# Performance work log

Measured on AMD Instinct MI355X. Metric: run time of the kernel, lower is better.

Reference implementation:

```python
import jax, jax.numpy as jnp
import numpy as np

DIM = 512
HEADS = 8
DH = 64          # dim_head = 512 // 8
M = 256          # num_landmarks = 512 // 2
PINV_ITERS = 6
N_PATCH = 40000
IN_DIM = 1024
NUM_CLASSES = 2
GRID = 200       # ceil(sqrt(40000)) -> exact square, add_length = 0


def layernorm(x, w, b, eps=1e-5):
    mu = x.mean(-1, keepdims=True)
    var = ((x - mu) ** 2).mean(-1, keepdims=True)
    return (x - mu) * jax.lax.rsqrt(var + eps) * w + b


def moore_penrose_pinv(x, iters=PINV_ITERS):
    # lucidrains nystrom-attention iterative pseudoinverse
    ax = jnp.abs(x)
    z = jnp.swapaxes(x, -1, -2) / (jnp.max(ax.sum(-1)) * jnp.max(ax.sum(-2)))
    I = jnp.eye(x.shape[-1], dtype=x.dtype)
    for _ in range(iters):
        xz = x @ z
        z = 0.25 * z @ (13 * I - xz @ (15 * I - xz @ (7 * I - xz)))
    return z


def depthwise_conv2d(x, w, pad):
    # x: (B,C,H,W); w: (C,1,kh,kw) torch-style OIHW depthwise kernel
    return jax.lax.conv_general_dilated(
        x, w, (1, 1), [(pad[0], pad[0]), (pad[1], pad[1])],
        dimension_numbers=('NCHW', 'OIHW', 'NCHW'),
        feature_group_count=x.shape[1])


def nystrom_attention(x, qkv_w, out_w, out_b, res_w):
    b, n, _ = x.shape
    pad = (M - n % M) % M
    xp = jnp.pad(x, ((0, 0), (pad, 0), (0, 0)))   # pad at FRONT of sequence
    N = n + pad
    qkv = xp @ qkv_w                              # (b,N,3*h*d), no bias
    q, k, v = jnp.split(qkv, 3, axis=-1)
    to_heads = lambda t: t.reshape(b, N, HEADS, DH).transpose(0, 2, 1, 3)
    q, k, v = to_heads(q), to_heads(k), to_heads(v)
    q = q * (DH ** -0.5)
    l = N // M
    q_l = q.reshape(b, HEADS, M, l, DH).mean(axis=3)   # (b,h,m,d) landmarks
    k_l = k.reshape(b, HEADS, M, l, DH).mean(axis=3)
    attn1 = jax.nn.softmax(jnp.einsum('bhid,bhjd->bhij', q, k_l), axis=-1)   # (b,h,N,m)
    attn2 = jax.nn.softmax(jnp.einsum('bhid,bhjd->bhij', q_l, k_l), axis=-1)  # (b,h,m,m)
    attn3 = jax.nn.softmax(jnp.einsum('bhid,bhjd->bhij', q_l, k), axis=-1)   # (b,h,m,N)
    out = (attn1 @ moore_penrose_pinv(attn2)) @ (attn3 @ v)                   # (b,h,N,d)
    out = out + depthwise_conv2d(v, res_w, (16, 0))    # residual depthwise conv (kernel 33x1)
    out = out.transpose(0, 2, 1, 3).reshape(b, N, HEADS * DH)[:, -n:]
    return out @ out_w + out_b


def ppeg(x, w7, b7, w5, b5, w3, b3, H, W):
    B, _, C = x.shape
    cls_t, feat = x[:, :1], x[:, 1:]
    f = feat.transpose(0, 2, 1).reshape(B, C, H, W)
    y = (f
         + depthwise_conv2d(f, w7, (3, 3)) + b7[None, :, None, None]
         + depthwise_conv2d(f, w5, (2, 2)) + b5[None, :, None, None]
         + depthwise_conv2d(f, w3, (1, 1)) + b3[None, :, None, None])
    y = y.reshape(B, C, H * W).transpose(0, 2, 1)
    return jnp.concatenate([cls_t, y], axis=1)


def setup_inputs() -> dict:
    key = jax.random.key(0)
    ks = iter(jax.random.split(key, 32))
    r = lambda shape, s=0.02: jax.random.normal(next(ks), shape, dtype=jnp.float32) * s
    inp = {
        'x': jax.random.normal(next(ks), (1, N_PATCH, IN_DIM), dtype=jnp.float32),
        'fc1_w': r((IN_DIM, DIM)), 'fc1_b': jnp.zeros((DIM,), jnp.float32),
        'cls_token': r((1, 1, DIM), 1e-6),
        'l1_norm_w': jnp.ones((DIM,), jnp.float32), 'l1_norm_b': jnp.zeros((DIM,), jnp.float32),
        'l1_qkv_w': r((DIM, 3 * HEADS * DH)), 'l1_out_w': r((HEADS * DH, DIM)),
        'l1_out_b': jnp.zeros((DIM,), jnp.float32), 'l1_res_w': r((HEADS, 1, 33, 1)),
        'p7_w': r((DIM, 1, 7, 7)), 'p7_b': jnp.zeros((DIM,), jnp.float32),
        'p5_w': r((DIM, 1, 5, 5)), 'p5_b': jnp.zeros((DIM,), jnp.float32),
        'p3_w': r((DIM, 1, 3, 3)), 'p3_b': jnp.zeros((DIM,), jnp.float32),
        'l2_norm_w': jnp.ones((DIM,), jnp.float32), 'l2_norm_b': jnp.zeros((DIM,), jnp.float32),
        'l2_qkv_w': r((DIM, 3 * HEADS * DH)), 'l2_out_w': r((HEADS * DH, DIM)),
        'l2_out_b': jnp.zeros((DIM,), jnp.float32), 'l2_res_w': r((HEADS, 1, 33, 1)),
        'norm_w': jnp.ones((DIM,), jnp.float32), 'norm_b': jnp.zeros((DIM,), jnp.float32),
        'fc2_w': r((DIM, NUM_CLASSES)), 'fc2_b': jnp.zeros((NUM_CLASSES,), jnp.float32),
    }
    return inp


def reference(x, fc1_w, fc1_b, cls_token,
              l1_norm_w, l1_norm_b, l1_qkv_w, l1_out_w, l1_out_b, l1_res_w,
              p7_w, p7_b, p5_w, p5_b, p3_w, p3_b,
              l2_norm_w, l2_norm_b, l2_qkv_w, l2_out_w, l2_out_b, l2_res_w,
              norm_w, norm_b, fc2_w, fc2_b):
    # _fc1: Linear + ReLU (dropout inactive at eval)
    h = jax.nn.relu(x @ fc1_w + fc1_b)            # (1, 40000, 512)
    # 40000 = 200*200 -> add_length = 0, no square padding needed
    B = h.shape[0]
    h = jnp.concatenate([jnp.broadcast_to(cls_token, (B, 1, DIM)), h], axis=1)
    # layer1: pre-norm Nystrom attention with residual
    h = h + nystrom_attention(layernorm(h, l1_norm_w, l1_norm_b), l1_qkv_w, l1_out_w, l1_out_b, l1_res_w)
    # PPEG positional mixing on the 200x200 token grid
    h = ppeg(h, p7_w, p7_b, p5_w, p5_b, p3_w, p3_b, GRID, GRID)
    # layer2
    h = h + nystrom_attention(layernorm(h, l2_norm_w, l2_norm_b), l2_qkv_w, l2_out_w, l2_out_b, l2_res_w)
    h = layernorm(h, norm_w, norm_b)
    cls_out = h[:, 0]
    logits = cls_out @ fc2_w + fc2_b              # (1, num_classes)
    return logits
```

## Files before the change

kernel.cpp:

```cpp
#include <hip/hip_runtime.h>
#include <hip/hip_bf16.h>

#define DIMC   512
#define HEADS  8
#define DH     64
#define MLM    256
#define NPATCH 40000
#define NTOK   40001
#define PADF   191
#define NSEQ   40192
#define NSEQP  40224
#define LWIN   157
#define INDIM  1024
#define GRID   200
#define CHUNKS 64
#define PER    628

typedef _Float16 h8 __attribute__((ext_vector_type(8)));
typedef _Float16 h4 __attribute__((ext_vector_type(4)));
typedef float    f4 __attribute__((ext_vector_type(4)));

#define WAVE_LDS_FENCE() asm volatile("s_waitcnt lgkmcnt(0)" ::: "memory")

__device__ __forceinline__ void gl_lds(const _Float16* g, _Float16* l) {
  __builtin_amdgcn_global_load_lds(
      (const __attribute__((address_space(1))) void*)g,
      (__attribute__((address_space(3))) void*)l, 16, 0, 0);
}

template<int NW, bool ISMAX>
__device__ __forceinline__ float blkRed(float v, float* s) {
  #pragma unroll
  for (int o = 32; o; o >>= 1) {
    float t = __shfl_down(v, o, 64);
    v = ISMAX ? fmaxf(v, t) : v + t;
  }
  int lane = threadIdx.x & 63, w = threadIdx.x >> 6;
  __syncthreads();
  if (lane == 0) s[w] = v;
  __syncthreads();
  float r = s[0];
  #pragma unroll
  for (int i = 1; i < NW; i++) r = ISMAX ? fmaxf(r, s[i]) : r + s[i];
  return r;
}

__global__ __launch_bounds__(512)
void k_set_cls(const float* __restrict__ cls, float* __restrict__ h) {
  h[threadIdx.x] = cls[threadIdx.x];
}

__global__ __launch_bounds__(256)
void k_f32_to_f16(const float* __restrict__ in, _Float16* __restrict__ out) {
  int i = blockIdx.x * 256 + threadIdx.x;
  float4 v = ((const float4*)in)[i];
  h4 o = {(_Float16)v.x, (_Float16)v.y, (_Float16)v.z, (_Float16)v.w};
  *(h4*)(out + (size_t)i * 4) = o;
}

__global__ __launch_bounds__(256)
void k_zpad(_Float16* q16, _Float16* k16, _Float16* v16) {
  int idx = blockIdx.x * 256 + threadIdx.x;
  int h = idx >> 11, r = (idx >> 6) & 31, d = idx & 63;
  size_t a = ((size_t)h * NSEQP + NSEQ + r) * 64 + d;
  q16[a] = (_Float16)0.f; k16[a] = (_Float16)0.f; v16[a] = (_Float16)0.f;
}

__global__ __launch_bounds__(256)
void k_wt16(const float* __restrict__ B, _Float16* __restrict__ Bt, int K, int N)
{
  __shared__ float tile[32][33];
  int kb = blockIdx.x * 32, nb = blockIdx.y * 32;
  int x = threadIdx.x & 31, y0 = threadIdx.x >> 5;
  #pragma unroll
  for (int yy = y0; yy < 32; yy += 8)
    tile[yy][x] = B[(size_t)(kb + yy) * N + nb + x];
  __syncthreads();
  #pragma unroll
  for (int yy = y0; yy < 32; yy += 8)
    Bt[(size_t)(nb + yy) * K + kb + x] = (_Float16)tile[x][yy];
}

__global__ __launch_bounds__(256)
void k_gemm16(const _Float16* __restrict__ A, const _Float16* __restrict__ Bt,
              const float* __restrict__ bias, float* __restrict__ C,
              _Float16* __restrict__ q16, _Float16* __restrict__ k16, _Float16* __restrict__ v16,
              int Mr, int K, int N, int flags)
{
  __shared__ __attribute__((aligned(16))) _Float16 As[128 * 32];
  __shared__ __attribute__((aligned(16))) _Float16 Bs[128 * 32];
  int bm = blockIdx.x * 128, bn = blockIdx.y * 128;
  int t = threadIdx.x;
  int lane = t & 63, w = t >> 6;
  int wm = (w >> 1) * 64, wn = (w & 1) * 64;
  int r = lane & 15, q = lane >> 4;
  int sub = lane >> 2;
  int kq = (lane & 3) * 8;

  const f4 zero = {0.f, 0.f, 0.f, 0.f};
  f4 acc[4][4];
  #pragma unroll
  for (int mi = 0; mi < 4; mi++)
    #pragma unroll
    for (int nj = 0; nj < 4; nj++) acc[mi][nj] = zero;

  for (int k0 = 0; k0 < K; k0 += 32) {
    #pragma unroll
    for (int c = 0; c < 2; c++) {
      int rowA = (w * 2 + c) * 16 + sub;
      int gmA = bm + rowA; if (gmA > Mr - 1) gmA = Mr - 1;
      gl_lds(A  + (size_t)gmA * K + k0 + kq,          As + (w * 2 + c) * 512);
      gl_lds(Bt + (size_t)(bn + rowA) * K + k0 + kq,  Bs + (w * 2 + c) * 512);
    }
    __syncthreads();
    h8 af[4], bf[4];
    #pragma unroll
    for (int i = 0; i < 4; i++) {
      af[i] = *(const h8*)(As + (wm + i * 16 + r) * 32 + q * 8);
      bf[i] = *(const h8*)(Bs + (wn + i * 16 + r) * 32 + q * 8);
    }
    #pragma unroll
    for (int mi = 0; mi < 4; mi++)
      #pragma unroll
      for (int nj = 0; nj < 4; nj++)
        acc[mi][nj] = __builtin_amdgcn_mfma_f32_16x16x32_f16(af[mi], bf[nj], acc[mi][nj], 0, 0, 0);
    __syncthreads();
  }
  #pragma unroll
  for (int mi = 0; mi < 4; mi++) {
    #pragma unroll
    for (int i = 0; i < 4; i++) {
      int gm = bm + wm + mi * 16 + q * 4 + i;
      if (gm >= Mr) continue;
      #pragma unroll
      for (int nj = 0; nj < 4; nj++) {
        int gn = bn + wn + nj * 16 + r;
        float v = acc[mi][nj][i];
        if (flags & 4) {
          int which = gn >> 9, hh = (gn >> 6) & 7, dd = gn & 63;
          _Float16* dst = (which == 0) ? q16 : (which == 1) ? k16 : v16;
          dst[((size_t)hh * NSEQP + gm) * 64 + dd] = (_Float16)v;
        } else {
          if (bias) v += bias[gn];
          if (flags & 2) v += C[(size_t)gm * N + gn];
          if (flags & 1) v = fmaxf(v, 0.f);
          C[(size_t)gm * N + gn] = v;
        }
      }
    }
  }
}

__global__ __launch_bounds__(256)
void k_ln_pad(const float* __restrict__ h, const float* __restrict__ w,
              const float* __restrict__ b, _Float16* __restrict__ xln)
{
  __shared__ float sbuf[8];
  int t = blockIdx.x;
  int tid = threadIdx.x;
  _Float16* out = xln + (size_t)t * DIMC;
  if (t < PADF) { out[tid] = (_Float16)0.f; out[tid + 256] = (_Float16)0.f; return; }
  const float* row = h + (size_t)(t - PADF) * DIMC;
  float x0 = row[tid], x1 = row[tid + 256];
  float mu = blkRed<4,false>(x0 + x1, sbuf) * (1.f / 512.f);
  float d0 = x0 - mu, d1 = x1 - mu;
  float var = blkRed<4,false>(d0 * d0 + d1 * d1, sbuf) * (1.f / 512.f);
  float rstd = rsqrtf(var + 1e-5f);
  out[tid]       = (_Float16)(d0 * rstd * w[tid]       + b[tid]);
  out[tid + 256] = (_Float16)(d1 * rstd * w[tid + 256] + b[tid + 256]);
}

__global__ __launch_bounds__(256)
void k_vt(const _Float16* __restrict__ v16, _Float16* __restrict__ vt16)
{
  __shared__ _Float16 tl[64][72];
  int h = blockIdx.y;
  int t0 = blockIdx.x * 64;
  for (int c = threadIdx.x; c < 512; c += 256) {
    int row = c >> 3, ch = (c & 7) * 8;
    h8 v = {};
    if (t0 + row < NSEQP)
      v = *(const h8*)(v16 + ((size_t)h * NSEQP + t0 + row) * 64 + ch);
    *(h8*)&tl[row][ch] = v;
  }
  __syncthreads();
  int d = threadIdx.x & 63, tg = (threadIdx.x >> 6) * 16;
  if (t0 + tg < NSEQP) {
    _Float16 tmp[16];
    #pragma unroll
    for (int k = 0; k < 16; k++) tmp[k] = tl[tg + k][d];
    *(h8*)(vt16 + ((size_t)h * 64 + d) * NSEQP + t0 + tg)     = *(h8*)tmp;
    *(h8*)(vt16 + ((size_t)h * 64 + d) * NSEQP + t0 + tg + 8) = *(h8*)(tmp + 8);
  }
}

__global__ __launch_bounds__(256)
void k_landmarks(const _Float16* __restrict__ q16, const _Float16* __restrict__ k16,
                 float* __restrict__ ql, float* __restrict__ kl,
                 _Float16* __restrict__ ql16, _Float16* __restrict__ kl16)
{
  __shared__ float red[2][16][64];
  int h = blockIdx.x >> 8, i = blockIdx.x & 255;
  int jg = threadIdx.x >> 4, d4 = (threadIdx.x & 15) * 4;
  const _Float16* qb = q16 + ((size_t)h * NSEQP + i * LWIN) * 64;
  const _Float16* kb = k16 + ((size_t)h * NSEQP + i * LWIN) * 64;
  float sq[4] = {}, sk[4] = {};
  for (int j = jg; j < LWIN; j += 16) {
    h4 qv = *(const h4*)(qb + j * 64 + d4);
    h4 kv = *(const h4*)(kb + j * 64 + d4);
    #pragma unroll
    for (int c = 0; c < 4; c++) { sq[c] += (float)qv[c]; sk[c] += (float)kv[c]; }
  }
  #pragma unroll
  for (int c = 0; c < 4; c++) { red[0][jg][d4 + c] = sq[c]; red[1][jg][d4 + c] = sk[c]; }
  __syncthreads();
  if (threadIdx.x < 64) {
    int d = threadIdx.x;
    float aq = 0.f, ak = 0.f;
    #pragma unroll
    for (int g = 0; g < 16; g++) { aq += red[0][g][d]; ak += red[1][g][d]; }
    aq *= (0.125f / (float)LWIN);
    ak *= (1.f / (float)LWIN);
    size_t o = ((size_t)h * MLM + i) * DH + d;
    ql[o] = aq; kl[o] = ak;
    ql16[o] = (_Float16)aq;
    kl16[o] = (_Float16)(ak * 0.125f);
  }
}

__global__ __launch_bounds__(256)
void k_attn2(const float* __restrict__ ql, const float* __restrict__ kl, float* __restrict__ a2)
{
  __shared__ float qrow[DH];
  __shared__ float sbuf[8];
  int h = blockIdx.x >> 8, i = blockIdx.x & 255;
  int j = threadIdx.x;
  if (j < DH) qrow[j] = ql[(h * MLM + i) * DH + j];
  __syncthreads();
  const float* krow = kl + (size_t)(h * MLM + j) * DH;
  float s = 0.f;
  #pragma unroll 16
  for (int d = 0; d < DH; d++) s += qrow[d] * krow[d];
  float mx = blkRed<4,true>(s, sbuf);
  float e = __expf(s - mx);
  float sum = blkRed<4,false>(e, sbuf);
  a2[((size_t)h * MLM + i) * MLM + j] = e / sum;
}

__global__ __launch_bounds__(256)
void k_pinv_init1(const float* __restrict__ a2, float* __restrict__ hmax)
{
  __shared__ float sbuf[8];
  int h = blockIdx.x;
  int j = threadIdx.x;
  const float* A = a2 + (size_t)h * MLM * MLM;
  float cs = 0.f, rs = 0.f;
  for (int i = 0; i < MLM; i++) cs += A[i * MLM + j];
  for (int k = 0; k < MLM; k++) rs += A[j * MLM + k];
  float rmax = blkRed<4,true>(rs, sbuf);
  float cmax = blkRed<4,true>(cs, sbuf);
  if (j == 0) { hmax[h * 2] = rmax; hmax[h * 2 + 1] = cmax; }
}

__global__ void k_pinv_init2(const float* __restrict__ hmax, float* __restrict__ scal)
{
  float rm = 0.f, cm = 0.f;
  for (int h = 0; h < HEADS; h++) { rm = fmaxf(rm, hmax[2*h]); cm = fmaxf(cm, hmax[2*h+1]); }
  scal[0] = 1.f / (rm * cm);
}

__global__ __launch_bounds__(256)
void k_pinv_prep(const float* __restrict__ a2, const float* __restrict__ scal,
                 _Float16* __restrict__ a2h, _Float16* __restrict__ a2l,
                 _Float16* __restrict__ zh,  _Float16* __restrict__ zl,
                 _Float16* __restrict__ zth, _Float16* __restrict__ ztl)
{
  __shared__ float tl[64][65];
  int h = blockIdx.x >> 4, tile = blockIdx.x & 15;
  int ti = (tile >> 2) * 64, tj = (tile & 3) * 64;
  float s = scal[0];
  int row = threadIdx.x >> 4, c4 = (threadIdx.x & 15) * 4;
  #pragma unroll
  for (int rr = 0; rr < 4; rr++) {
    int rloc = rr * 16 + row;
    f4 v = *(const f4*)(a2 + ((size_t)h * MLM + ti + rloc) * MLM + tj + c4);
    h4 hi, lo, zhi, zlo;
    #pragma unroll
    for (int c = 0; c < 4; c++) {
      hi[c] = (_Float16)v[c];
      lo[c] = (_Float16)(v[c] - (float)hi[c]);
      float zv = v[c] * s;
      zhi[c] = (_Float16)zv;
      zlo[c] = (_Float16)(zv - (float)zhi[c]);
      tl[rloc][c4 + c] = zv;
    }
    size_t idx = ((size_t)h * MLM + ti + rloc) * MLM + tj + c4;
    *(h4*)(a2h + idx) = hi;  *(h4*)(a2l + idx) = lo;
    *(h4*)(zth + idx) = zhi; *(h4*)(ztl + idx) = zlo;
  }
  __syncthreads();
// ... 147 lines not shown
    f4 S[4][2];
    #pragma unroll
    for (int mt = 0; mt < 4; mt++) { S[mt][0] = zero; S[mt][1] = zero; }
    #pragma unroll
    for (int nt = 0; nt < 2; nt++) {
      h8 b0 = *(const h8*)(kh + (size_t)(tt + nt * 16 + r) * 64 + q * 8);
      h8 b1 = *(const h8*)(kh + (size_t)(tt + nt * 16 + r) * 64 + 32 + q * 8);
      #pragma unroll
      for (int mt = 0; mt < 4; mt++) {
        S[mt][nt] = __builtin_amdgcn_mfma_f32_16x16x32_f16(af[mt][0], b0, S[mt][nt], 0, 0, 0);
        S[mt][nt] = __builtin_amdgcn_mfma_f32_16x16x32_f16(af[mt][1], b1, S[mt][nt], 0, 0, 0);
      }
    }
    if (tb == 19) {
      #pragma unroll
      for (int nt = 0; nt < 2; nt++) {
        bool valid = (tb * 32 + nt * 16 + r) < PER;
        #pragma unroll
        for (int mt = 0; mt < 4; mt++)
          #pragma unroll
          for (int i = 0; i < 4; i++)
            S[mt][nt][i] = valid ? S[mt][nt][i] : -1e30f;
      }
    }
    #pragma unroll
    for (int mt = 0; mt < 4; mt++) {
      float nm[4], al[4], ls[4];
      #pragma unroll
      for (int i = 0; i < 4; i++) {
        nm[i] = fmaxf(S[mt][0][i], S[mt][1][i]);
        #pragma unroll
        for (int o = 1; o < 16; o <<= 1) nm[i] = fmaxf(nm[i], __shfl_xor(nm[i], o, 64));
        nm[i] = fmaxf(nm[i], mrun[mt][i]);
        al[i] = __expf(mrun[mt][i] - nm[i]);
        mrun[mt][i] = nm[i];
        float p0 = __expf(S[mt][0][i] - nm[i]);
        float p1 = __expf(S[mt][1][i] - nm[i]);
        S[mt][0][i] = p0; S[mt][1][i] = p1;
        ls[i] = p0 + p1;
        #pragma unroll
        for (int o = 1; o < 16; o <<= 1) ls[i] += __shfl_xor(ls[i], o, 64);
        lrun[mt][i] = lrun[mt][i] * al[i] + ls[i];
      }
      #pragma unroll
      for (int nd = 0; nd < 4; nd++)
        #pragma unroll
        for (int i = 0; i < 4; i++) acc[mt][nd][i] *= al[i];
      #pragma unroll
      for (int nt = 0; nt < 2; nt++)
        #pragma unroll
        for (int i = 0; i < 4; i++)
          Pw[(mt * 16 + q * 4 + i) * 40 + nt * 16 + r] = (_Float16)S[mt][nt][i];
    }
    WAVE_LDS_FENCE();
    h8 bv[4];
    #pragma unroll
    for (int nd = 0; nd < 4; nd++)
      bv[nd] = *(const h8*)(vh + (size_t)(nd * 16 + r) * NSEQP + tt + q * 8);
    #pragma unroll
    for (int mt = 0; mt < 4; mt++) {
      h8 ap = *(const h8*)(Pw + (mt * 16 + r) * 40 + q * 8);
      #pragma unroll
      for (int nd = 0; nd < 4; nd++)
        acc[mt][nd] = __builtin_amdgcn_mfma_f32_16x16x32_f16(ap, bv[nd], acc[mt][nd], 0, 0, 0);
    }
    WAVE_LDS_FENCE();
  }
  int cidx = h * CHUNKS + c;
  #pragma unroll
  for (int mt = 0; mt < 4; mt++) {
    int rowb = m0 + mt * 16 + q * 4;
    if (r == 0) {
      #pragma unroll
      for (int i = 0; i < 4; i++) {
        pm[(size_t)cidx * MLM + rowb + i] = mrun[mt][i];
        ps[(size_t)cidx * MLM + rowb + i] = lrun[mt][i];
      }
    }
    #pragma unroll
    for (int nd = 0; nd < 4; nd++)
      #pragma unroll
      for (int i = 0; i < 4; i++)
        pacc[((size_t)cidx * MLM + rowb + i) * 64 + nd * 16 + r] = acc[mt][nd][i];
  }
}

__global__ __launch_bounds__(64)
void k_attn3_reduce(const float* __restrict__ pm, const float* __restrict__ ps,
                    const float* __restrict__ pacc,
                    _Float16* __restrict__ avth, _Float16* __restrict__ avtl)
{
  int h = blockIdx.x >> 8, i = blockIdx.x & 255;
  int d = threadIdx.x;
  float m = -1e30f;
  for (int c = 0; c < CHUNKS; c++) m = fmaxf(m, pm[(h * CHUNKS + c) * MLM + i]);
  float l = 0.f, a = 0.f;
  for (int c = 0; c < CHUNKS; c++) {
    int idx = (h * CHUNKS + c) * MLM + i;
    float w = __expf(pm[idx] - m);
    l += ps[idx] * w;
    a += pacc[(size_t)idx * DH + d] * w;
  }
  float v = a / l;
  _Float16 hi = (_Float16)v;
  size_t o = ((size_t)h * DH + d) * MLM + i;
  avth[o] = hi;
  avtl[o] = (_Float16)(v - (float)hi);
}

__global__ __launch_bounds__(256)
void k_conv(const _Float16* __restrict__ v16, const float* __restrict__ rw,
            _Float16* __restrict__ xat)
{
  __shared__ float tl[160][64];
  int h = blockIdx.y;
  int t0 = PADF + blockIdx.x * 128;
  for (int c = threadIdx.x; c < 160 * 16; c += 256) {
    int row = c >> 4, d4 = (c & 15) * 4;
    int ts = t0 - 16 + row;
    f4 val = {0.f, 0.f, 0.f, 0.f};
    if (ts >= 0 && ts < NSEQ) {
      h4 hv = *(const h4*)(v16 + ((size_t)h * NSEQP + ts) * 64 + d4);
      val[0] = (float)hv[0]; val[1] = (float)hv[1]; val[2] = (float)hv[2]; val[3] = (float)hv[3];
    }
    *(f4*)&tl[row][d4] = val;
  }
  __syncthreads();
  float wt[33];
  #pragma unroll
  for (int tap = 0; tap < 33; tap++) wt[tap] = rw[h * 33 + tap];
  int d4 = (threadIdx.x & 15) * 4, r0 = threadIdx.x >> 4;
  #pragma unroll
  for (int k = 0; k < 8; k++) {
    int r = k * 16 + r0;
    int t = t0 + r;
    f4 acc = {0.f, 0.f, 0.f, 0.f};
    #pragma unroll
    for (int tap = 0; tap < 33; tap++) {
      f4 vv = *(const f4*)&tl[r + tap][d4];
      acc[0] += wt[tap] * vv[0]; acc[1] += wt[tap] * vv[1];
      acc[2] += wt[tap] * vv[2]; acc[3] += wt[tap] * vv[3];
    }
    if (t < NSEQ) {
      h4 o = {(_Float16)acc[0], (_Float16)acc[1], (_Float16)acc[2], (_Float16)acc[3]};
      *(h4*)(xat + (size_t)t * DIMC + h * 64 + d4) = o;
    }
  }
}

__global__ __launch_bounds__(256)
void k_attn1(const _Float16* __restrict__ q16, const _Float16* __restrict__ kl16,
             const _Float16* __restrict__ w2t16, _Float16* __restrict__ xat)
{
  __shared__ __attribute__((aligned(16))) _Float16 Pl[4][16 * 264];
  int h = blockIdx.y;
  int t0 = PADF + blockIdx.x * 64;
  int tid = threadIdx.x, lane = tid & 63, w = tid >> 6;
  int r = lane & 15, q = lane >> 4;
  int tq = t0 + w * 16 + r; if (tq > NSEQ - 1) tq = NSEQ - 1;
  const _Float16* qrow = q16 + ((size_t)h * NSEQP + tq) * 64;
  h8 bq0 = *(const h8*)(qrow + q * 8);
  h8 bq1 = *(const h8*)(qrow + 32 + q * 8);
  const _Float16* klh = kl16 + (size_t)h * MLM * 64;
  const f4 zero = {0.f, 0.f, 0.f, 0.f};
  f4 S[16];
  #pragma unroll
  for (int nj = 0; nj < 16; nj++) {
    h8 a0 = *(const h8*)(klh + (size_t)(nj * 16 + r) * 64 + q * 8);
    h8 a1 = *(const h8*)(klh + (size_t)(nj * 16 + r) * 64 + 32 + q * 8);
    f4 s = zero;
    s = __builtin_amdgcn_mfma_f32_16x16x32_f16(a0, bq0, s, 0, 0, 0);
    s = __builtin_amdgcn_mfma_f32_16x16x32_f16(a1, bq1, s, 0, 0, 0);
    S[nj] = s;
  }
  float mx = -1e30f;
  #pragma unroll
  for (int nj = 0; nj < 16; nj++)
    #pragma unroll
    for (int i = 0; i < 4; i++) mx = fmaxf(mx, S[nj][i]);
  mx = fmaxf(mx, __shfl_xor(mx, 16, 64));
  mx = fmaxf(mx, __shfl_xor(mx, 32, 64));
  float l = 0.f;
  _Float16* Pw = &Pl[w][0];
  #pragma unroll
  for (int nj = 0; nj < 16; nj++) {
    h4 pv;
    #pragma unroll
    for (int i = 0; i < 4; i++) {
      float p = __expf(S[nj][i] - mx);
      l += p;
      pv[i] = (_Float16)p;
    }
    *(h4*)(Pw + r * 264 + nj * 16 + q * 4) = pv;
  }
  l += __shfl_xor(l, 16, 64);
  l += __shfl_xor(l, 32, 64);
  float linv = 1.f / l;
  WAVE_LDS_FENCE();
  const _Float16* w2h = w2t16 + (size_t)h * 64 * 256;
  f4 o4[4];
  #pragma unroll
  for (int nd = 0; nd < 4; nd++) o4[nd] = zero;
  #pragma unroll
  for (int ks = 0; ks < 8; ks++) {
    h8 ap = *(const h8*)(Pw + r * 264 + ks * 32 + q * 8);
    #pragma unroll
    for (int nd = 0; nd < 4; nd++) {
      h8 bw = *(const h8*)(w2h + (size_t)(nd * 16 + r) * 256 + ks * 32 + q * 8);
      o4[nd] = __builtin_amdgcn_mfma_f32_16x16x32_f16(ap, bw, o4[nd], 0, 0, 0);
    }
  }
  WAVE_LDS_FENCE();
  float* ow = (float*)Pw;
  float li[4];
  #pragma unroll
  for (int i = 0; i < 4; i++) li[i] = __shfl(linv, q * 4 + i, 16);
  #pragma unroll
  for (int nd = 0; nd < 4; nd++)
    #pragma unroll
    for (int i = 0; i < 4; i++)
      ow[(q * 4 + i) * 66 + nd * 16 + r] = o4[nd][i] * li[i];
  WAVE_LDS_FENCE();
  #pragma unroll
  for (int c = 0; c < 2; c++) {
    int e = lane + c * 64;
    int row = e >> 3, ch = (e & 7) * 8;
    int t = t0 + w * 16 + row;
    if (t < NSEQ) {
      float* src = ow + row * 66 + ch;
      _Float16* dst = xat + (size_t)t * DIMC + h * 64 + ch;
      h8 cv = *(h8*)dst;
      h8 outv;
      #pragma unroll
      for (int k = 0; k < 8; k++) outv[k] = (_Float16)(src[k] + (float)cv[k]);
      *(h8*)dst = outv;
    }
  }
}

__global__ __launch_bounds__(256)
void k_transpose_fw(const float* __restrict__ h, float* __restrict__ g)
{
  __shared__ float tile[32][33];
  int pb = blockIdx.x * 32, cb = blockIdx.y * 32;
  int x = threadIdx.x & 31, y0 = threadIdx.x >> 5;
  #pragma unroll
  for (int yy = y0; yy < 32; yy += 8)
    tile[yy][x] = h[(size_t)(1 + pb + yy) * DIMC + cb + x];
  __syncthreads();
  #pragma unroll
  for (int yy = y0; yy < 32; yy += 8)
    g[(size_t)(cb + yy) * NPATCH + pb + x] = tile[x][yy];
}

__global__ __launch_bounds__(256)
void k_ppeg(const float* __restrict__ g,
            const float* __restrict__ w7, const float* __restrict__ b7,
            const float* __restrict__ w5, const float* __restrict__ b5,
            const float* __restrict__ w3, const float* __restrict__ b3,
            float* __restrict__ o)
{
  __shared__ float tl[22][22];
  int c = blockIdx.y;
  int ty0 = (blockIdx.x / 13) * 16, tx0 = (blockIdx.x % 13) * 16;
  const float* gc = g + (size_t)c * NPATCH;
  for (int e = threadIdx.x; e < 22 * 22; e += 256) {
    int yy = e / 22, xx = e % 22;
    int y = ty0 - 3 + yy, x = tx0 - 3 + xx;
    tl[yy][xx] = (y >= 0 && y < GRID && x >= 0 && x < GRID) ? gc[y * GRID + x] : 0.f;
  }
  __syncthreads();
  int ly = threadIdx.x >> 4, lx = threadIdx.x & 15;
  int y = ty0 + ly, x = tx0 + lx;
  if (y >= GRID || x >= GRID) return;
  float acc = tl[ly + 3][lx + 3] + b7[c] + b5[c] + b3[c];
  #pragma unroll
  for (int ky = 0; ky < 7; ky++)
    #pragma unroll
    for (int kx = 0; kx < 7; kx++)
      acc += w7[c * 49 + ky * 7 + kx] * tl[ly + ky][lx + kx];
  #pragma unroll
  for (int ky = 0; ky < 5; ky++)
    #pragma unroll
    for (int kx = 0; kx < 5; kx++)
      acc += w5[c * 25 + ky * 5 + kx] * tl[ly + 1 + ky][lx + 1 + kx];
  #pragma unroll
  for (int ky = 0; ky < 3; ky++)
    #pragma unroll
    for (int kx = 0; kx < 3; kx++)
      acc += w3[c * 9 + ky * 3 + kx] * tl[ly + 2 + ky][lx + 2 + kx];
  o[(size_t)c * NPATCH + y * GRID + x] = acc;
}

__global__ __launch_bounds__(256)
void k_transpose_bw(const float* __restrict__ g, float* __restrict__ h)
{
  __shared__ float tile[32][33];
  int pb = blockIdx.x * 32, cb = blockIdx.y * 32;
  int x = threadIdx.x & 31, y0 = threadIdx.x >> 5;
  #pragma unroll
  for (int yy = y0; yy < 32; yy += 8)
    tile[yy][x] = g[(size_t)(cb + yy) * NPATCH + pb + x];
  __syncthreads();
  #pragma unroll
  for (int yy = y0; yy < 32; yy += 8)
    h[(size_t)(1 + pb + yy) * DIMC + cb + x] = tile[x][yy];
}

__global__ __launch_bounds__(512)
void k_final(const float* __restrict__ h, const float* __restrict__ nw, const float* __restrict__ nb,
             const float* __restrict__ fw, const float* __restrict__ fb, float* __restrict__ out)
{
  __shared__ float sbuf[8];
  int d = threadIdx.x;
  float x = h[d];
  float mu = blkRed<8,false>(x, sbuf) * (1.f / 512.f);
  float dd = x - mu;
  float var = blkRed<8,false>(dd * dd, sbuf) * (1.f / 512.f);
  float cls = dd * rsqrtf(var + 1e-5f) * nw[d] + nb[d];
  float l0 = blkRed<8,false>(cls * fw[d * 2 + 0], sbuf);
  float l1 = blkRed<8,false>(cls * fw[d * 2 + 1], sbuf);
  if (d == 0) { out[0] = l0 + fb[0]; out[1] = l1 + fb[1]; }
}

struct Pair4 { _Float16 *h, *l, *th, *tl; };
struct WsPtrs {
  float *h, *ql, *kl, *a2, *hmax, *scal, *pm, *ps, *pacc;
  _Float16 *xat16, *q16, *k16, *v16, *vt16, *ql16, *kl16, *x16;
  _Float16 *a2h, *a2l, *avth, *avtl;
  Pair4 zA, zB, xz, u, u2, w2;
};

static void attention_layer(const WsPtrs& P,
                            const float* nw, const float* nb, const _Float16* qkvw16,
                            const _Float16* ow16, const float* ob, const float* rw,
                            hipStream_t stream)
{
  k_zpad<<<64, 256, 0, stream>>>(P.q16, P.k16, P.v16);
  k_ln_pad<<<NSEQ, 256, 0, stream>>>(P.h, nw, nb, P.xat16);
  k_gemm16<<<dim3(NSEQ / 128, 1536 / 128), 256, 0, stream>>>(
      P.xat16, qkvw16, nullptr, nullptr, P.q16, P.k16, P.v16, NSEQ, DIMC, 3 * DIMC, 4);
  k_vt<<<dim3(629, HEADS), 256, 0, stream>>>(P.v16, P.vt16);
  k_landmarks<<<HEADS * MLM, 256, 0, stream>>>(P.q16, P.k16, P.ql, P.kl, P.ql16, P.kl16);
  k_attn2<<<HEADS * MLM, 256, 0, stream>>>(P.ql, P.kl, P.a2);
  k_pinv_init1<<<HEADS, 256, 0, stream>>>(P.a2, P.hmax);
  k_pinv_init2<<<1, 1, 0, stream>>>(P.hmax, P.scal);
  k_pinv_prep<<<HEADS * 16, 256, 0, stream>>>(P.a2, P.scal,
      P.a2h, P.a2l, P.zA.h, P.zA.l, P.zA.th, P.zA.tl);
  Pair4 z = P.zA, zn = P.zB;
  for (int it = 0; it < 6; it++) {
    k_pbmm<<<dim3(16, HEADS), 256, 0, stream>>>(P.a2h, P.a2l, z.th, z.tl,
        nullptr, nullptr, P.xz.h, P.xz.l, P.xz.th, P.xz.tl, MLM, 1.f, 0.f);
    k_pbmm<<<dim3(16, HEADS), 256, 0, stream>>>(P.xz.h, P.xz.l, P.xz.th, P.xz.tl,
        P.xz.h, P.xz.l, nullptr, nullptr, P.u.th, P.u.tl, MLM, -1.f, 7.f);
    k_pbmm<<<dim3(16, HEADS), 256, 0, stream>>>(P.xz.h, P.xz.l, P.u.th, P.u.tl,
        P.xz.h, P.xz.l, nullptr, nullptr, P.u2.th, P.u2.tl, MLM, -1.f, 15.f);
    k_pbmm<<<dim3(16, HEADS), 256, 0, stream>>>(z.h, z.l, P.u2.th, P.u2.tl,
        z.h, z.l, zn.h, zn.l, zn.th, zn.tl, MLM, -0.25f, 3.25f);
    Pair4 t = z; z = zn; zn = t;
  }
  k_attn3<<<dim3(CHUNKS, HEADS), 256, 0, stream>>>(P.ql16, P.k16, P.vt16, P.pm, P.ps, P.pacc);
  k_attn3_reduce<<<HEADS * MLM, 64, 0, stream>>>(P.pm, P.ps, P.pacc, P.avth, P.avtl);
  k_pbmm<<<dim3(4, HEADS), 256, 0, stream>>>(z.h, z.l, P.avth, P.avtl,
      nullptr, nullptr, nullptr, nullptr, P.w2.th, P.w2.tl, DH, 1.f, 0.f);
  k_conv<<<dim3(313, HEADS), 256, 0, stream>>>(P.v16, rw, P.xat16);
  k_attn1<<<dim3(626, HEADS), 256, 0, stream>>>(P.q16, P.kl16, P.w2.th, P.xat16);
  k_gemm16<<<dim3((NTOK + 127) / 128, DIMC / 128), 256, 0, stream>>>(
      P.xat16 + (size_t)PADF * DIMC, ow16, ob, P.h, nullptr, nullptr, nullptr, NTOK, DIMC, DIMC, 2);
}

extern "C" void kernel_launch(void* const* d_in, const int* in_sizes, int n_in,
                              void* d_out, int out_size, void* d_ws, size_t ws_size,
                              hipStream_t stream)
{
  const float* x      = (const float*)d_in[0];
  const float* fc1_w  = (const float*)d_in[1];
  const float* fc1_b  = (const float*)d_in[2];
  const float* cls    = (const float*)d_in[3];
  const float* l1_nw  = (const float*)d_in[4];
  const float* l1_nb  = (const float*)d_in[5];
  const float* l1_qkv = (const float*)d_in[6];
  const float* l1_ow  = (const float*)d_in[7];
  const float* l1_ob  = (const float*)d_in[8];
  const float* l1_rw  = (const float*)d_in[9];
  const float* p7w    = (const float*)d_in[10];
  const float* p7b    = (const float*)d_in[11];
  const float* p5w    = (const float*)d_in[12];
  const float* p5b    = (const float*)d_in[13];
  const float* p3w    = (const float*)d_in[14];
  const float* p3b    = (const float*)d_in[15];
  const float* l2_nw  = (const float*)d_in[16];
  const float* l2_nb  = (const float*)d_in[17];
  const float* l2_qkv = (const float*)d_in[18];
  const float* l2_ow  = (const float*)d_in[19];
  const float* l2_ob  = (const float*)d_in[20];
  const float* l2_rw  = (const float*)d_in[21];
  const float* nw     = (const float*)d_in[22];
  const float* nb     = (const float*)d_in[23];
  const float* fc2w   = (const float*)d_in[24];
  const float* fc2b   = (const float*)d_in[25];
  float* out = (float*)d_out;

  float* W = (float*)d_ws;
  WsPtrs P;
  size_t off = 0;
  P.h     = W + off;               off += 20480512ull;
  P.xat16 = (_Float16*)(W + off);  off += 10289152ull;
  float* R0 = W + off;
  P.q16   = (_Float16*)R0;
  P.k16   = P.q16 + 20594688ull;
  P.v16   = P.k16 + 20594688ull;
  P.vt16  = P.v16 + 20594688ull;
  P.x16   = P.q16;
  off += 41189376ull;
  P.ql    = W + off; off += 131072;
  P.kl    = W + off; off += 131072;
  P.ql16  = (_Float16*)(W + off); off += 65536;
  P.kl16  = (_Float16*)(W + off); off += 65536;
  P.a2    = W + off; off += 524288;
  _Float16* HP = (_Float16*)(W + off);
  size_t ho = 0;
  P.a2h = HP + ho; ho += 524288; P.a2l = HP + ho; ho += 524288;
  auto alloc4 = [&](Pair4& p, size_t n) {
    p.h = HP + ho; ho += n; p.l = HP + ho; ho += n;
    p.th = HP + ho; ho += n; p.tl = HP + ho; ho += n;
  };
  alloc4(P.zA, 524288); alloc4(P.zB, 524288); alloc4(P.xz, 524288);
  alloc4(P.u, 524288);  alloc4(P.u2, 524288);
  alloc4(P.w2, 131072);
  P.avth = HP + ho; ho += 131072; P.avtl = HP + ho; ho += 131072;
  off += (ho + 1) / 2;
  P.hmax  = W + off; P.scal = P.hmax + 16; off += 32;
  P.pm    = W + off; off += 131072;
  P.ps    = W + off; off += 131072;
  P.pacc  = W + off; off += 8388608;
  _Float16* fc1t  = (_Float16*)(W + off);
  _Float16* qkv1t = fc1t  + 524288;
  _Float16* out1t = qkv1t + 786432;
  _Float16* qkv2t = out1t + 262144;
  _Float16* out2t = qkv2t + 786432;

  k_wt16<<<dim3(INDIM / 32, DIMC / 32), 256, 0, stream>>>(fc1_w, fc1t, INDIM, DIMC);
  k_wt16<<<dim3(DIMC / 32, 1536 / 32), 256, 0, stream>>>(l1_qkv, qkv1t, DIMC, 1536);
  k_wt16<<<dim3(DIMC / 32, DIMC / 32), 256, 0, stream>>>(l1_ow, out1t, DIMC, DIMC);
  k_wt16<<<dim3(DIMC / 32, 1536 / 32), 256, 0, stream>>>(l2_qkv, qkv2t, DIMC, 1536);
  k_wt16<<<dim3(DIMC / 32, DIMC / 32), 256, 0, stream>>>(l2_ow, out2t, DIMC, DIMC);

  k_f32_to_f16<<<NPATCH * INDIM / 1024, 256, 0, stream>>>(x, P.x16);
  k_gemm16<<<dim3((NPATCH + 127) / 128, DIMC / 128), 256, 0, stream>>>(
      P.x16, fc1t, fc1_b, P.h + DIMC, nullptr, nullptr, nullptr, NPATCH, INDIM, DIMC, 1);
  k_set_cls<<<1, 512, 0, stream>>>(cls, P.h);

  attention_layer(P, l1_nw, l1_nb, qkv1t, out1t, l1_ob, l1_rw, stream);

  float* fgrid = R0;
  float* cout  = R0 + 20480000ull;
  k_transpose_fw<<<dim3(NPATCH / 32, DIMC / 32), 256, 0, stream>>>(P.h, fgrid);
  k_ppeg<<<dim3(13 * 13, DIMC), 256, 0, stream>>>(fgrid, p7w, p7b, p5w, p5b, p3w, p3b, cout);
  k_transpose_bw<<<dim3(NPATCH / 32, DIMC / 32), 256, 0, stream>>>(cout, P.h);

  attention_layer(P, l2_nw, l2_nb, qkv2t, out2t, l2_ob, l2_rw, stream);

  k_final<<<1, 512, 0, stream>>>(P.h, nw, nb, fc2w, fc2b, out);
}
```

Measured before the change: 2.474 ms.

## Widen GEMM tile to 128x256 with vectorized epilogue; split attn1 softmax into halves

The fp16 MFMA GEMM now computes a 128x256 output tile per block (8 accumulators per wave in N). Swapping the MFMA operand order makes each lane hold four consecutive columns, so the epilogue writes 4-wide vector stores instead of scalar ones. In k_attn1 the scores are computed twice: once for the max, then again in two halves that feed the P·W2 MFMA directly. This removes the 16-register S array and halves the LDS buffer for P. The tradeoffs are more accumulator registers and fewer blocks in the GEMMs, plus recomputed QK MFMAs in attn1.

Result: slower. 2.820 ms (+14.0%).

```diff
diff --git a/kernel.cpp b/kernel.cpp
--- a/kernel.cpp
+++ b/kernel.cpp
@@ -88,64 +88,74 @@
               int Mr, int K, int N, int flags)
 {
   __shared__ __attribute__((aligned(16))) _Float16 As[128 * 32];
-  __shared__ __attribute__((aligned(16))) _Float16 Bs[128 * 32];
-  int bm = blockIdx.x * 128, bn = blockIdx.y * 128;
+  __shared__ __attribute__((aligned(16))) _Float16 Bs[256 * 32];
+  int bm = blockIdx.x * 128, bn = blockIdx.y * 256;
   int t = threadIdx.x;
   int lane = t & 63, w = t >> 6;
-  int wm = (w >> 1) * 64, wn = (w & 1) * 64;
+  int wm = (w >> 1) * 64, wn = (w & 1) * 128;
   int r = lane & 15, q = lane >> 4;
   int sub = lane >> 2;
   int kq = (lane & 3) * 8;
 
   const f4 zero = {0.f, 0.f, 0.f, 0.f};
-  f4 acc[4][4];
+  f4 acc[4][8];
   #pragma unroll
   for (int mi = 0; mi < 4; mi++)
     #pragma unroll
-    for (int nj = 0; nj < 4; nj++) acc[mi][nj] = zero;
+    for (int nj = 0; nj < 8; nj++) acc[mi][nj] = zero;
 
   for (int k0 = 0; k0 < K; k0 += 32) {
     #pragma unroll
     for (int c = 0; c < 2; c++) {
-      int rowA = (w * 2 + c) * 16 + sub;
+      int rowA = (c * 4 + w) * 16 + sub;
       int gmA = bm + rowA; if (gmA > Mr - 1) gmA = Mr - 1;
-      gl_lds(A  + (size_t)gmA * K + k0 + kq,          As + (w * 2 + c) * 512);
-      gl_lds(Bt + (size_t)(bn + rowA) * K + k0 + kq,  Bs + (w * 2 + c) * 512);
+      gl_lds(A + (size_t)gmA * K + k0 + kq, As + (c * 4 + w) * 512);
+    }
+    #pragma unroll
+    for (int c = 0; c < 4; c++) {
+      int rowB = (c * 4 + w) * 16 + sub;
+      gl_lds(Bt + (size_t)(bn + rowB) * K + k0 + kq, Bs + (c * 4 + w) * 512);
     }
     __syncthreads();
-    h8 af[4], bf[4];
-    #pragma unroll
-    for (int i = 0; i < 4; i++) {
+    h8 af[4], bf[8];
+    #pragma unroll
+    for (int i = 0; i < 4; i++)
       af[i] = *(const h8*)(As + (wm + i * 16 + r) * 32 + q * 8);
-      bf[i] = *(const h8*)(Bs + (wn + i * 16 + r) * 32 + q * 8);
-    }
+    #pragma unroll
+    for (int j = 0; j < 8; j++)
+      bf[j] = *(const h8*)(Bs + (wn + j * 16 + r) * 32 + q * 8);
     #pragma unroll
     for (int mi = 0; mi < 4; mi++)
       #pragma unroll
-      for (int nj = 0; nj < 4; nj++)
-        acc[mi][nj] = __builtin_amdgcn_mfma_f32_16x16x32_f16(af[mi], bf[nj], acc[mi][nj], 0, 0, 0);
+      for (int nj = 0; nj < 8; nj++)
+        acc[mi][nj] = __builtin_amdgcn_mfma_f32_16x16x32_f16(bf[nj], af[mi], acc[mi][nj], 0, 0, 0);
     __syncthreads();
   }
   #pragma unroll
   for (int mi = 0; mi < 4; mi++) {
-    #pragma unroll
-    for (int i = 0; i < 4; i++) {
-      int gm = bm + wm + mi * 16 + q * 4 + i;
-      if (gm >= Mr) continue;
-      #pragma unroll
-      for (int nj = 0; nj < 4; nj++) {
-        int gn = bn + wn + nj * 16 + r;
-        float v = acc[mi][nj][i];
-        if (flags & 4) {
-          int which = gn >> 9, hh = (gn >> 6) & 7, dd = gn & 63;
-          _Float16* dst = (which == 0) ? q16 : (which == 1) ? k16 : v16;
-          dst[((size_t)hh * NSEQP + gm) * 64 + dd] = (_Float16)v;
-        } else {
-          if (bias) v += bias[gn];
-          if (flags & 2) v += C[(size_t)gm * N + gn];
-          if (flags & 1) v = fmaxf(v, 0.f);
-          C[(size_t)gm * N + gn] = v;
+    int gm = bm + wm + mi * 16 + r;
+    if (gm >= Mr) continue;
+    #pragma unroll
+    for (int nj = 0; nj < 8; nj++) {
+      int gn = bn + wn + nj * 16 + q * 4;
+      f4 v = acc[mi][nj];
+      if (flags & 4) {
+        int which = gn >> 9, hh = (gn >> 6) & 7, dd = gn & 63;
+        _Float16* dst = (which == 0) ? q16 : (which == 1) ? k16 : v16;
+        h4 o = {(_Float16)v[0], (_Float16)v[1], (_Float16)v[2], (_Float16)v[3]};
+        *(h4*)(dst + ((size_t)hh * NSEQP + gm) * 64 + dd) = o;
+      } else {
+        if (bias) {
+          v[0] += bias[gn]; v[1] += bias[gn + 1];
+          v[2] += bias[gn + 2]; v[3] += bias[gn + 3];
         }
+        float* cp = C + (size_t)gm * N + gn;
+        if (flags & 2) { f4 cv = *(const f4*)cp; v += cv; }
+        if (flags & 1) {
+          v[0] = fmaxf(v[0], 0.f); v[1] = fmaxf(v[1], 0.f);
+          v[2] = fmaxf(v[2], 0.f); v[3] = fmaxf(v[3], 0.f);
+        }
+        *(f4*)cp = v;
       }
     }
   }
@@ -599,7 +609,7 @@
 void k_attn1(const _Float16* __restrict__ q16, const _Float16* __restrict__ kl16,
              const _Float16* __restrict__ w2t16, _Float16* __restrict__ xat)
 {
-  __shared__ __attribute__((aligned(16))) _Float16 Pl[4][16 * 264];
+  __shared__ __attribute__((aligned(16))) _Float16 Pl[4][16 * 136];
   int h = blockIdx.y;
   int t0 = PADF + blockIdx.x * 64;
   int tid = threadIdx.x, lane = tid & 63, w = tid >> 6;
@@ -610,7 +620,7 @@
   h8 bq1 = *(const h8*)(qrow + 32 + q * 8);
   const _Float16* klh = kl16 + (size_t)h * MLM * 64;
   const f4 zero = {0.f, 0.f, 0.f, 0.f};
-  f4 S[16];
+  float mx = -1e30f;
   #pragma unroll
   for (int nj = 0; nj < 16; nj++) {
     h8 a0 = *(const h8*)(klh + (size_t)(nj * 16 + r) * 64 + q * 8);
@@ -618,46 +628,50 @@
     f4 s = zero;
     s = __builtin_amdgcn_mfma_f32_16x16x32_f16(a0, bq0, s, 0, 0, 0);
     s = __builtin_amdgcn_mfma_f32_16x16x32_f16(a1, bq1, s, 0, 0, 0);
-    S[nj] = s;
-  }
-  float mx = -1e30f;
-  #pragma unroll
-  for (int nj = 0; nj < 16; nj++)
-    #pragma unroll
-    for (int i = 0; i < 4; i++) mx = fmaxf(mx, S[nj][i]);
+    mx = fmaxf(mx, fmaxf(fmaxf(s[0], s[1]), fmaxf(s[2], s[3])));
+  }
   mx = fmaxf(mx, __shfl_xor(mx, 16, 64));
   mx = fmaxf(mx, __shfl_xor(mx, 32, 64));
   float l = 0.f;
   _Float16* Pw = &Pl[w][0];
-  #pragma unroll
-  for (int nj = 0; nj < 16; nj++) {
-    h4 pv;
-    #pragma unroll
-    for (int i = 0; i < 4; i++) {
-      float p = __expf(S[nj][i] - mx);
-      l += p;
-      pv[i] = (_Float16)p;
-    }
-    *(h4*)(Pw + r * 264 + nj * 16 + q * 4) = pv;
+  const _Float16* w2h = w2t16 + (size_t)h * 64 * 256;
+  f4 o4[4];
+  #pragma unroll
+  for (int nd = 0; nd < 4; nd++) o4[nd] = zero;
+  #pragma unroll
+  for (int half = 0; half < 2; half++) {
+    #pragma unroll
+    for (int nj8 = 0; nj8 < 8; nj8++) {
+      int nj = half * 8 + nj8;
+      h8 a0 = *(const h8*)(klh + (size_t)(nj * 16 + r) * 64 + q * 8);
+      h8 a1 = *(const h8*)(klh + (size_t)(nj * 16 + r) * 64 + 32 + q * 8);
+      f4 s = zero;
+      s = __builtin_amdgcn_mfma_f32_16x16x32_f16(a0, bq0, s, 0, 0, 0);
+      s = __builtin_amdgcn_mfma_f32_16x16x32_f16(a1, bq1, s, 0, 0, 0);
+      h4 pv;
+      #pragma unroll
+      for (int i = 0; i < 4; i++) {
+        float p = __expf(s[i] - mx);
+        l += p;
+        pv[i] = (_Float16)p;
+      }
+      *(h4*)(Pw + r * 136 + nj8 * 16 + q * 4) = pv;
+    }
+    WAVE_LDS_FENCE();
+    #pragma unroll
+    for (int ks = 0; ks < 4; ks++) {
+      h8 ap = *(const h8*)(Pw + r * 136 + ks * 32 + q * 8);
+      #pragma unroll
+      for (int nd = 0; nd < 4; nd++) {
+        h8 bw = *(const h8*)(w2h + (size_t)(nd * 16 + r) * 256 + half * 128 + ks * 32 + q * 8);
+        o4[nd] = __builtin_amdgcn_mfma_f32_16x16x32_f16(ap, bw, o4[nd], 0, 0, 0);
+      }
+    }
+    WAVE_LDS_FENCE();
   }
   l += __shfl_xor(l, 16, 64);
   l += __shfl_xor(l, 32, 64);
   float linv = 1.f / l;
-  WAVE_LDS_FENCE();
-  const _Float16* w2h = w2t16 + (size_t)h * 64 * 256;
-  f4 o4[4];
-  #pragma unroll
-  for (int nd = 0; nd < 4; nd++) o4[nd] = zero;
-  #pragma unroll
-  for (int ks = 0; ks < 8; ks++) {
-    h8 ap = *(const h8*)(Pw + r * 264 + ks * 32 + q * 8);
-    #pragma unroll
-    for (int nd = 0; nd < 4; nd++) {
-      h8 bw = *(const h8*)(w2h + (size_t)(nd * 16 + r) * 256 + ks * 32 + q * 8);
-      o4[nd] = __builtin_amdgcn_mfma_f32_16x16x32_f16(ap, bw, o4[nd], 0, 0, 0);
-    }
-  }
-  WAVE_LDS_FENCE();
   float* ow = (float*)Pw;
   float li[4];
   #pragma unroll
@@ -785,7 +799,7 @@
 {
   k_zpad<<<64, 256, 0, stream>>>(P.q16, P.k16, P.v16);
   k_ln_pad<<<NSEQ, 256, 0, stream>>>(P.h, nw, nb, P.xat16);
-  k_gemm16<<<dim3(NSEQ / 128, 1536 / 128), 256, 0, stream>>>(
+  k_gemm16<<<dim3(NSEQ / 128, 1536 / 256), 256, 0, stream>>>(
       P.xat16, qkvw16, nullptr, nullptr, P.q16, P.k16, P.v16, NSEQ, DIMC, 3 * DIMC, 4);
   k_vt<<<dim3(629, HEADS), 256, 0, stream>>>(P.v16, P.vt16);
   k_landmarks<<<HEADS * MLM, 256, 0, stream>>>(P.q16, P.k16, P.ql, P.kl, P.ql16, P.kl16);
@@ -812,7 +826,7 @@
       nullptr, nullptr, nullptr, nullptr, P.w2.th, P.w2.tl, DH, 1.f, 0.f);
   k_conv<<<dim3(313, HEADS), 256, 0, stream>>>(P.v16, rw, P.xat16);
   k_attn1<<<dim3(626, HEADS), 256, 0, stream>>>(P.q16, P.kl16, P.w2.th, P.xat16);
-  k_gemm16<<<dim3((NTOK + 127) / 128, DIMC / 128), 256, 0, stream>>>(
+  k_gemm16<<<dim3((NTOK + 127) / 128, DIMC / 256), 256, 0, stream>>>(
       P.xat16 + (size_t)PADF * DIMC, ow16, ob, P.h, nullptr, nullptr, nullptr, NTOK, DIMC, DIMC, 2);
 }
 
@@ -894,7 +908,7 @@
   k_wt16<<<dim3(DIMC / 32, DIMC / 32), 256, 0, stream>>>(l2_ow, out2t, DIMC, DIMC);
 
   k_f32_to_f16<<<NPATCH * INDIM / 1024, 256, 0, stream>>>(x, P.x16);
-  k_gemm16<<<dim3((NPATCH + 127) / 128, DIMC / 128), 256, 0, stream>>>(
+  k_gemm16<<<dim3((NPATCH + 127) / 128, DIMC / 256), 256, 0, stream>>>(
       P.x16, fc1t, fc1_b, P.h + DIMC, nullptr, nullptr, nullptr, NPATCH, INDIM, DIMC, 1);
   k_set_cls<<<1, 512, 0, stream>>>(cls, P.h);
 
```

## Restructure attn1 as flash-style online softmax and vectorize GEMM epilogue stores

Applied to the files above, without the earlier changes.

k_attn1 now has each wave handle 64 query rows instead of 16, walking the 256 landmarks in 32-wide blocks with an online softmax. This reuses each landmark-key and W2 fragment across four query tiles and cuts the grid from 626 to 157 blocks per head. The generic GEMM swaps its MFMA operands so each lane holds four consecutive columns, which turns the epilogue into vectorized f4/h4 loads and stores instead of scalar strided writes. The costs are extra cross-lane shuffles for the per-row max and sum, rescaling of the accumulators, more registers per wave, and an fp16 round-trip of the output before the residual add.

New measurement: 2.317 ms. -6.3%, faster.

```diff
diff --git a/kernel.cpp b/kernel.cpp
--- a/kernel.cpp
+++ b/kernel.cpp
@@ -123,29 +123,31 @@
     for (int mi = 0; mi < 4; mi++)
       #pragma unroll
       for (int nj = 0; nj < 4; nj++)
-        acc[mi][nj] = __builtin_amdgcn_mfma_f32_16x16x32_f16(af[mi], bf[nj], acc[mi][nj], 0, 0, 0);
+        acc[mi][nj] = __builtin_amdgcn_mfma_f32_16x16x32_f16(bf[nj], af[mi], acc[mi][nj], 0, 0, 0);
     __syncthreads();
   }
   #pragma unroll
   for (int mi = 0; mi < 4; mi++) {
-    #pragma unroll
-    for (int i = 0; i < 4; i++) {
-      int gm = bm + wm + mi * 16 + q * 4 + i;
-      if (gm >= Mr) continue;
-      #pragma unroll
-      for (int nj = 0; nj < 4; nj++) {
-        int gn = bn + wn + nj * 16 + r;
-        float v = acc[mi][nj][i];
-        if (flags & 4) {
-          int which = gn >> 9, hh = (gn >> 6) & 7, dd = gn & 63;
-          _Float16* dst = (which == 0) ? q16 : (which == 1) ? k16 : v16;
-          dst[((size_t)hh * NSEQP + gm) * 64 + dd] = (_Float16)v;
-        } else {
-          if (bias) v += bias[gn];
-          if (flags & 2) v += C[(size_t)gm * N + gn];
-          if (flags & 1) v = fmaxf(v, 0.f);
-          C[(size_t)gm * N + gn] = v;
+    int gm = bm + wm + mi * 16 + r;
+    if (gm >= Mr) continue;
+    #pragma unroll
+    for (int nj = 0; nj < 4; nj++) {
+      int gn = bn + wn + nj * 16 + q * 4;
+      f4 v = acc[mi][nj];
+      if (flags & 4) {
+        int which = gn >> 9, hh = (gn >> 6) & 7, dd = gn & 63;
+        _Float16* dst = (which == 0) ? q16 : (which == 1) ? k16 : v16;
+        h4 o = {(_Float16)v[0], (_Float16)v[1], (_Float16)v[2], (_Float16)v[3]};
+        *(h4*)(dst + ((size_t)hh * NSEQP + gm) * 64 + dd) = o;
+      } else {
+        if (bias) { f4 bv = *(const f4*)(bias + gn); v += bv; }
+        float* cp = C + (size_t)gm * N + gn;
+        if (flags & 2) { f4 cv = *(const f4*)cp; v += cv; }
+        if (flags & 1) {
+          v[0] = fmaxf(v[0], 0.f); v[1] = fmaxf(v[1], 0.f);
+          v[2] = fmaxf(v[2], 0.f); v[3] = fmaxf(v[3], 0.f);
         }
+        *(f4*)cp = v;
       }
     }
   }
@@ -599,89 +601,124 @@
 void k_attn1(const _Float16* __restrict__ q16, const _Float16* __restrict__ kl16,
              const _Float16* __restrict__ w2t16, _Float16* __restrict__ xat)
 {
-  __shared__ __attribute__((aligned(16))) _Float16 Pl[4][16 * 264];
+  __shared__ __attribute__((aligned(16))) _Float16 Pl[4][64 * 40];
   int h = blockIdx.y;
-  int t0 = PADF + blockIdx.x * 64;
+  int t0 = blockIdx.x * 256;
   int tid = threadIdx.x, lane = tid & 63, w = tid >> 6;
   int r = lane & 15, q = lane >> 4;
-  int tq = t0 + w * 16 + r; if (tq > NSEQ - 1) tq = NSEQ - 1;
-  const _Float16* qrow = q16 + ((size_t)h * NSEQP + tq) * 64;
-  h8 bq0 = *(const h8*)(qrow + q * 8);
-  h8 bq1 = *(const h8*)(qrow + 32 + q * 8);
+  int m0 = w * 64;
+  const _Float16* qh  = q16  + (size_t)h * NSEQP * 64;
   const _Float16* klh = kl16 + (size_t)h * MLM * 64;
+  const _Float16* w2h = w2t16 + (size_t)h * 64 * 256;
+  _Float16* Pw = &Pl[w][0];
+
+  h8 af[4][2];
+  #pragma unroll
+  for (int mt = 0; mt < 4; mt++)
+    #pragma unroll
+    for (int ks = 0; ks < 2; ks++)
+      af[mt][ks] = *(const h8*)(qh + (size_t)(t0 + m0 + mt * 16 + r) * 64 + ks * 32 + q * 8);
+
   const f4 zero = {0.f, 0.f, 0.f, 0.f};
-  f4 S[16];
-  #pragma unroll
-  for (int nj = 0; nj < 16; nj++) {
-    h8 a0 = *(const h8*)(klh + (size_t)(nj * 16 + r) * 64 + q * 8);
-    h8 a1 = *(const h8*)(klh + (size_t)(nj * 16 + r) * 64 + 32 + q * 8);
-    f4 s = zero;
-    s = __builtin_amdgcn_mfma_f32_16x16x32_f16(a0, bq0, s, 0, 0, 0);
-    s = __builtin_amdgcn_mfma_f32_16x16x32_f16(a1, bq1, s, 0, 0, 0);
-    S[nj] = s;
-  }
-  float mx = -1e30f;
-  #pragma unroll
-  for (int nj = 0; nj < 16; nj++)
-    #pragma unroll
-    for (int i = 0; i < 4; i++) mx = fmaxf(mx, S[nj][i]);
-  mx = fmaxf(mx, __shfl_xor(mx, 16, 64));
-  mx = fmaxf(mx, __shfl_xor(mx, 32, 64));
-  float l = 0.f;
-  _Float16* Pw = &Pl[w][0];
-  #pragma unroll
-  for (int nj = 0; nj < 16; nj++) {
-    h4 pv;
-    #pragma unroll
-    for (int i = 0; i < 4; i++) {
-      float p = __expf(S[nj][i] - mx);
-      l += p;
-      pv[i] = (_Float16)p;
-    }
-    *(h4*)(Pw + r * 264 + nj * 16 + q * 4) = pv;
-  }
-  l += __shfl_xor(l, 16, 64);
-  l += __shfl_xor(l, 32, 64);
-  float linv = 1.f / l;
-  WAVE_LDS_FENCE();
-  const _Float16* w2h = w2t16 + (size_t)h * 64 * 256;
-  f4 o4[4];
-  #pragma unroll
-  for (int nd = 0; nd < 4; nd++) o4[nd] = zero;
-  #pragma unroll
-  for (int ks = 0; ks < 8; ks++) {
-    h8 ap = *(const h8*)(Pw + r * 264 + ks * 32 + q * 8);
-    #pragma unroll
-    for (int nd = 0; nd < 4; nd++) {
-      h8 bw = *(const h8*)(w2h + (size_t)(nd * 16 + r) * 256 + ks * 32 + q * 8);
-      o4[nd] = __builtin_amdgcn_mfma_f32_16x16x32_f16(ap, bw, o4[nd], 0, 0, 0);
-    }
-  }
-  WAVE_LDS_FENCE();
-  float* ow = (float*)Pw;
-  float li[4];
-  #pragma unroll
-  for (int i = 0; i < 4; i++) li[i] = __shfl(linv, q * 4 + i, 16);
-  #pragma unroll
-  for (int nd = 0; nd < 4; nd++)
-    #pragma unroll
-    for (int i = 0; i < 4; i++)
-      ow[(q * 4 + i) * 66 + nd * 16 + r] = o4[nd][i] * li[i];
-  WAVE_LDS_FENCE();
-  #pragma unroll
-  for (int c = 0; c < 2; c++) {
-    int e = lane + c * 64;
-    int row = e >> 3, ch = (e & 7) * 8;
-    int t = t0 + w * 16 + row;
-    if (t < NSEQ) {
-      float* src = ow + row * 66 + ch;
-      _Float16* dst = xat + (size_t)t * DIMC + h * 64 + ch;
-      h8 cv = *(h8*)dst;
-      h8 outv;
-      #pragma unroll
-      for (int k = 0; k < 8; k++) outv[k] = (_Float16)(src[k] + (float)cv[k]);
-      *(h8*)dst = outv;
-    }
+  f4 acc[4][4];
+  float mrun[4][4], lrun[4][4];
+  #pragma unroll
+  for (int mt = 0; mt < 4; mt++) {
+    #pragma unroll
+    for (int nd = 0; nd < 4; nd++) acc[mt][nd] = zero;
+    #pragma unroll
+    for (int i = 0; i < 4; i++) { mrun[mt][i] = -1e30f; lrun[mt][i] = 0.f; }
+  }
+
+  for (int tb = 0; tb < 8; tb++) {
+    int tt = tb * 32;
+    f4 S[4][2];
+    #pragma unroll
+    for (int mt = 0; mt < 4; mt++) { S[mt][0] = zero; S[mt][1] = zero; }
+    #pragma unroll
+    for (int nt = 0; nt < 2; nt++) {
+      h8 b0 = *(const h8*)(klh + (size_t)(tt + nt * 16 + r) * 64 + q * 8);
+      h8 b1 = *(const h8*)(klh + (size_t)(tt + nt * 16 + r) * 64 + 32 + q * 8);
+      #pragma unroll
+      for (int mt = 0; mt < 4; mt++) {
+        S[mt][nt] = __builtin_amdgcn_mfma_f32_16x16x32_f16(af[mt][0], b0, S[mt][nt], 0, 0, 0);
+        S[mt][nt] = __builtin_amdgcn_mfma_f32_16x16x32_f16(af[mt][1], b1, S[mt][nt], 0, 0, 0);
+      }
+    }
+    #pragma unroll
+    for (int mt = 0; mt < 4; mt++) {
+      float nm[4], al[4], ls[4];
+      #pragma unroll
+      for (int i = 0; i < 4; i++) {
+        nm[i] = fmaxf(S[mt][0][i], S[mt][1][i]);
+        #pragma unroll
+        for (int o = 1; o < 16; o <<= 1) nm[i] = fmaxf(nm[i], __shfl_xor(nm[i], o, 64));
+        nm[i] = fmaxf(nm[i], mrun[mt][i]);
+        al[i] = __expf(mrun[mt][i] - nm[i]);
+        mrun[mt][i] = nm[i];
+        float p0 = __expf(S[mt][0][i] - nm[i]);
+        float p1 = __expf(S[mt][1][i] - nm[i]);
+        S[mt][0][i] = p0; S[mt][1][i] = p1;
+        ls[i] = p0 + p1;
+        #pragma unroll
+        for (int o = 1; o < 16; o <<= 1) ls[i] += __shfl_xor(ls[i], o, 64);
+        lrun[mt][i] = lrun[mt][i] * al[i] + ls[i];
+      }
+      #pragma unroll
+      for (int nd = 0; nd < 4; nd++)
+        #pragma unroll
+        for (int i = 0; i < 4; i++) acc[mt][nd][i] *= al[i];
+      #pragma unroll
+      for (int nt = 0; nt < 2; nt++)
+        #pragma unroll
+        for (int i = 0; i < 4; i++)
+          Pw[(mt * 16 + q * 4 + i) * 40 + nt * 16 + r] = (_Float16)S[mt][nt][i];
+    }
+    WAVE_LDS_FENCE();
+    h8 bw[4];
+    #pragma unroll
+    for (int nd = 0; nd < 4; nd++)
+      bw[nd] = *(const h8*)(w2h + (size_t)(nd * 16 + r) * 256 + tt + q * 8);
+    #pragma unroll
+    for (int mt = 0; mt < 4; mt++) {
+      h8 ap = *(const h8*)(Pw + (mt * 16 + r) * 40 + q * 8);
+      #pragma unroll
+      for (int nd = 0; nd < 4; nd++)
+        acc[mt][nd] = __builtin_amdgcn_mfma_f32_16x16x32_f16(ap, bw[nd], acc[mt][nd], 0, 0, 0);
+    }
+    WAVE_LDS_FENCE();
+  }
+  #pragma unroll
+  for (int half = 0; half < 2; half++) {
+    #pragma unroll
+    for (int mt2 = 0; mt2 < 2; mt2++) {
+      int mt = half * 2 + mt2;
+      float li[4];
+      #pragma unroll
+      for (int i = 0; i < 4; i++) li[i] = 1.f / lrun[mt][i];
+      #pragma unroll
+      for (int nd = 0; nd < 4; nd++)
+        #pragma unroll
+        for (int i = 0; i < 4; i++)
+          Pw[(mt2 * 16 + q * 4 + i) * 72 + nd * 16 + r] = (_Float16)(acc[mt][nd][i] * li[i]);
+    }
+    WAVE_LDS_FENCE();
+    #pragma unroll
+    for (int c = 0; c < 4; c++) {
+      int row = c * 8 + (lane >> 3);
+      int ch = (lane & 7) * 8;
+      int t = t0 + m0 + half * 32 + row;
+      if (t >= PADF) {
+        _Float16* dst = xat + (size_t)t * DIMC + h * 64 + ch;
+        h8 cv = *(h8*)dst;
+        h8 pv = *(const h8*)(Pw + row * 72 + ch);
+        h8 o;
+        #pragma unroll
+        for (int k = 0; k < 8; k++) o[k] = (_Float16)((float)cv[k] + (float)pv[k]);
+        *(h8*)dst = o;
+      }
+    }
+    WAVE_LDS_FENCE();
   }
 }
 
@@ -811,7 +848,7 @@
   k_pbmm<<<dim3(4, HEADS), 256, 0, stream>>>(z.h, z.l, P.avth, P.avtl,
       nullptr, nullptr, nullptr, nullptr, P.w2.th, P.w2.tl, DH, 1.f, 0.f);
   k_conv<<<dim3(313, HEADS), 256, 0, stream>>>(P.v16, rw, P.xat16);
-  k_attn1<<<dim3(626, HEADS), 256, 0, stream>>>(P.q16, P.kl16, P.w2.th, P.xat16);
+  k_attn1<<<dim3(157, HEADS), 256, 0, stream>>>(P.q16, P.kl16, P.w2.th, P.xat16);
   k_gemm16<<<dim3((NTOK + 127) / 128, DIMC / 128), 256, 0, stream>>>(
       P.xat16 + (size_t)PADF * DIMC, ow16, ob, P.h, nullptr, nullptr, nullptr, NTOK, DIMC, DIMC, 2);
 }
```
